# Performance work log

Hardware: AMD Instinct MI355X
Metric: run time of the kernel (lower is better)

## Reference

```python
import jax, jax.numpy as jnp
import numpy as np

B, D, L, N, M, K = 256, 512, 196, 1024, 512, 10000  # batch, context, num_ctx, hidden, embed, vocab


def setup_inputs() -> dict:
    key = jax.random.key(0)
    ks = jax.random.split(key, 20)
    r = lambda k, s: jax.random.normal(k, s, dtype=jnp.float32) * 0.02
    return {
        "a_i": jax.random.normal(ks[0], (B, D, L), dtype=jnp.float32),
        "inp": jax.random.normal(ks[1], (B, 1, K), dtype=jnp.float32),
        "hn_prev": jax.random.normal(ks[2], (B, 1, N), dtype=jnp.float32),
        "cn_prev": jax.random.normal(ks[3], (B, 1, N), dtype=jnp.float32),
        "f_att_w": r(ks[4], (N + D,)),  # Linear(n+D -> 1), stored as a vector
        "f_att_b": r(ks[5], (1,)),
        "gate_w": r(ks[6], (N,)),       # Linear(n -> 1)
        "gate_b": r(ks[7], (1,)),
        "E_w": r(ks[8], (M, K)),        # torch Linear weight [out, in]
        "E_b": r(ks[9], (M,)),
        "W_ih": r(ks[10], (4 * N, D + N + M)),  # LSTM input->hidden (i,f,g,o)
        "W_hh": r(ks[11], (4 * N, N)),
        "b_ih": r(ks[12], (4 * N,)),
        "b_hh": r(ks[13], (4 * N,)),
        "Lh_w": r(ks[14], (M, N)),
        "Lh_b": r(ks[15], (M,)),
        "Lz_w": r(ks[16], (M, D)),
        "Lz_b": r(ks[17], (M,)),
        "Lo_w": r(ks[18], (K, M)),
        "Lo_b": r(ks[19], (K,)),
    }


def reference(a_i, inp, hn_prev, cn_prev,
              f_att_w, f_att_b, gate_w, gate_b,
              E_w, E_b, W_ih, W_hh, b_ih, b_hh,
              Lh_w, Lh_b, Lz_w, Lz_b, Lo_w, Lo_b):
    h = hn_prev[:, 0]  # [B, N]
    c = cn_prev[:, 0]  # [B, N]
    # --- additive attention: the 196-iteration torch loop batched into one einsum ---
    # cat((a_i[:,:,i], h)) @ f_att_w splits into the a-part and h-part of the weight.
    w_a, w_h = f_att_w[:D], f_att_w[D:]
    e = jnp.einsum('bdl,d->bl', a_i, w_a) + (h @ w_h)[:, None] + f_att_b  # [B, L]
    alpha = jax.nn.softmax(e, axis=1)                                     # [B, L]
    beta = jax.nn.sigmoid(h @ gate_w + gate_b)                            # [B]
    z = beta[:, None] * jnp.einsum('bl,bdl->bd', alpha, a_i)              # [B, D]
    # --- word embedding ---
    w_emb = inp[:, 0] @ E_w.T + E_b                                       # [B, M]
    # --- single-step LSTM (PyTorch gate order i, f, g, o) ---
    x = jnp.concatenate([w_emb, h, z], axis=1)                            # [B, M+N+D]
    gates = x @ W_ih.T + b_ih + h @ W_hh.T + b_hh                         # [B, 4N]
    i_g, f_g, g_g, o_g = jnp.split(gates, 4, axis=1)
    cn = jax.nn.sigmoid(f_g) * c + jax.nn.sigmoid(i_g) * jnp.tanh(g_g)
    hn = jax.nn.sigmoid(o_g) * jnp.tanh(cn)
    # --- output projection ---
    deep_out = w_emb + (hn @ Lh_w.T + Lh_b) + (z @ Lz_w.T + Lz_b)         # [B, M]
    p_yt = deep_out @ Lo_w.T + Lo_b                                       # [B, K]
    return (p_yt[:, None, :], hn[:, None, :], cn[:, None, :], alpha[:, None, :])
```

## Files before the change

### kernel.cpp

```cpp
#include <hip/hip_runtime.h>
#include <hip/hip_bf16.h>
#include <math.h>

#define BB 256
#define DD 512
#define LL 196
#define NN 1024
#define MM 512
#define KK 10000

#define OUT_PY 0
#define OUT_HN ((size_t)2560000)
#define OUT_CN ((size_t)2822144)
#define OUT_AL ((size_t)3084288)

#define OFF_PE     ((size_t)0)
#define OFF_BETA   ((size_t)802816)
#define OFF_Z      ((size_t)803072)
#define OFF_EMB    ((size_t)934144)
#define OFF_DEEP   ((size_t)1065216)
#define OFF_EMBP   ((size_t)1196288)
#define OFF_GATESP ((size_t)2244864)
#define OFF_DP     ((size_t)10633472)

typedef __attribute__((ext_vector_type(8))) short short8v;
typedef __attribute__((ext_vector_type(4))) float f32x4;

__device__ __forceinline__ unsigned short f2bf(float f) {
    unsigned int u = __builtin_bit_cast(unsigned int, f);
    u += 0x7fffu + ((u >> 16) & 1u);
    return (unsigned short)(u >> 16);
}

__device__ __forceinline__ short8v stage8(const float* __restrict__ p, bool ok,
                                          int kbase, int Ktot) {
    short8v v;
    if (ok && (kbase + 7 < Ktot)) {
        const float4 x = *(const float4*)(p + kbase);
        const float4 y = *(const float4*)(p + kbase + 4);
        v[0] = (short)f2bf(x.x); v[1] = (short)f2bf(x.y);
        v[2] = (short)f2bf(x.z); v[3] = (short)f2bf(x.w);
        v[4] = (short)f2bf(y.x); v[5] = (short)f2bf(y.y);
        v[6] = (short)f2bf(y.z); v[7] = (short)f2bf(y.w);
    } else {
#pragma unroll
        for (int i = 0; i < 8; ++i) {
            const int k = kbase + i;
            v[i] = (short)f2bf((ok && k < Ktot) ? p[k] : 0.f);
        }
    }
    return v;
}

struct GSrc { const float* A; int lda; const float* B; int ldb; int ktn; int K; };

__device__ __forceinline__ void gemm_body(
    const int bx, const int by, const int bz, const int rowBlocks,
    const GSrc s1, const GSrc s2,
    float* __restrict__ C, const int ldc, const int Ncols,
    const int ktPerSplit, const float* __restrict__ bias,
    short (*As)[64][72], short (*Bs)[64][72])
{
    const int t = threadIdx.x;
    const int row0 = bx * 64;
    const int col0 = by * 64;
    const int ktTot = s1.ktn + s2.ktn;
    const int kt0 = bz * ktPerSplit;
    const int nk = min(ktTot, kt0 + ktPerSplit) - kt0;

    const int sr = t >> 2;
    const int sk = (t & 3) << 4;
    const int bc = col0 + sr;
    const bool bok = (bc < Ncols);
    const float* aP1 = s1.A + (size_t)(row0 + sr) * s1.lda;
    const float* bP1 = s1.B + (size_t)(bok ? bc : 0) * s1.ldb;
    const float* aP2 = s2.A ? (s2.A + (size_t)(row0 + sr) * s2.lda) : aP1;
    const float* bP2 = s2.A ? (s2.B + (size_t)(bok ? bc : 0) * s2.ldb) : bP1;

    const int l = t & 63, w = t >> 6;
    const int wrow = (w >> 1) * 32, wcol = (w & 1) * 32;
    const int lr = l & 15, g = l >> 4, g8 = g * 8;

    f32x4 acc[2][2] = {};

    short8v sa0, sa1, sb0, sb1;
    {
        const int ktg = kt0;
        const float* aR; const float* bR; int kk, Kt;
        if (ktg < s1.ktn) { aR = aP1; bR = bP1; kk = (ktg << 6) + sk; Kt = s1.K; }
        else              { aR = aP2; bR = bP2; kk = ((ktg - s1.ktn) << 6) + sk; Kt = s2.K; }
        sa0 = stage8(aR, true, kk, Kt);  sa1 = stage8(aR, true, kk + 8, Kt);
        sb0 = stage8(bR, bok,  kk, Kt);  sb1 = stage8(bR, bok,  kk + 8, Kt);
    }
    *(short8v*)&As[0][sr][sk] = sa0; *(short8v*)&As[0][sr][sk + 8] = sa1;
    *(short8v*)&Bs[0][sr][sk] = sb0; *(short8v*)&Bs[0][sr][sk + 8] = sb1;
    __syncthreads();

    int cur = 0;
    for (int kt = 0; kt < nk; ++kt) {
        const bool more = (kt + 1 < nk);
        if (more) {
            const int ktg = kt0 + kt + 1;
            const float* aR; const float* bR; int kk, Kt;
            if (ktg < s1.ktn) { aR = aP1; bR = bP1; kk = (ktg << 6) + sk; Kt = s1.K; }
            else              { aR = aP2; bR = bP2; kk = ((ktg - s1.ktn) << 6) + sk; Kt = s2.K; }
            sa0 = stage8(aR, true, kk, Kt);  sa1 = stage8(aR, true, kk + 8, Kt);
            sb0 = stage8(bR, bok,  kk, Kt);  sb1 = stage8(bR, bok,  kk + 8, Kt);
        }
#pragma unroll
        for (int ks = 0; ks < 2; ++ks) {
            const int ko = ks * 32 + g8;
            short8v a0 = *(const short8v*)&As[cur][wrow + lr][ko];
            short8v a1 = *(const short8v*)&As[cur][wrow + 16 + lr][ko];
            short8v b0 = *(const short8v*)&Bs[cur][wcol + lr][ko];
            short8v b1 = *(const short8v*)&Bs[cur][wcol + 16 + lr][ko];
            acc[0][0] = __builtin_amdgcn_mfma_f32_16x16x32_bf16(a0, b0, acc[0][0], 0, 0, 0);
            acc[0][1] = __builtin_amdgcn_mfma_f32_16x16x32_bf16(a0, b1, acc[0][1], 0, 0, 0);
            acc[1][0] = __builtin_amdgcn_mfma_f32_16x16x32_bf16(a1, b0, acc[1][0], 0, 0, 0);
            acc[1][1] = __builtin_amdgcn_mfma_f32_16x16x32_bf16(a1, b1, acc[1][1], 0, 0, 0);
        }
        if (more) {
            *(short8v*)&As[cur ^ 1][sr][sk] = sa0;
            *(short8v*)&As[cur ^ 1][sr][sk + 8] = sa1;
            *(short8v*)&Bs[cur ^ 1][sr][sk] = sb0;
            *(short8v*)&Bs[cur ^ 1][sr][sk + 8] = sb1;
        }
        __syncthreads();
        cur ^= 1;
    }

    float* Cp = C + (size_t)bz * ((size_t)rowBlocks * 64) * ldc;
#pragma unroll
    for (int m = 0; m < 2; ++m)
#pragma unroll
        for (int n = 0; n < 2; ++n)
#pragma unroll
            for (int j = 0; j < 4; ++j) {
                const int r = row0 + wrow + m * 16 + g * 4 + j;
                const int c = col0 + wcol + n * 16 + lr;
                if (c < Ncols) {
                    float v = acc[m][n][j];
                    if (bias) v += bias[c];
                    Cp[(size_t)r * ldc + c] = v;
                }
            }
}

__global__ __launch_bounds__(256) void k1_atte_emb_gatesh(
    const float* __restrict__ a_i, const float* __restrict__ f_att_w,
    float* __restrict__ pe,
    const float* __restrict__ inp, const float* __restrict__ E_w,
    float* __restrict__ embp,
    const float* __restrict__ h, const float* __restrict__ W_ih,
    const float* __restrict__ W_hh, float* __restrict__ gatesp)
{
    __shared__ __align__(16) unsigned char smem[36864];
    const int bid = blockIdx.x;
    const int t = threadIdx.x;

    if (bid < 4096) {
        float* pw = (float*)smem;
        const int b = bid >> 4, ch = bid & 15;
        const int w = t >> 6, lane = t & 63;
        const int d0 = ch * 32 + w * 8;
        const float* base = a_i + ((size_t)b * DD + d0) * LL;
        float e4[4] = {0.f, 0.f, 0.f, 0.f};
        if (lane < 49) {
            float4 rbuf[8];
#pragma unroll
            for (int i = 0; i < 8; ++i)
                rbuf[i] = *(const float4*)(base + (size_t)i * LL + lane * 4);
#pragma unroll
            for (int i = 0; i < 8; ++i) {
                const float wa = f_att_w[d0 + i];
                e4[0] += rbuf[i].x * wa; e4[1] += rbuf[i].y * wa;
                e4[2] += rbuf[i].z * wa; e4[3] += rbuf[i].w * wa;
            }
            *(float4*)&pw[w * 200 + lane * 4] = *(const float4*)e4;
        }
        __syncthreads();
        if (t < LL) {
            const float s = pw[t] + pw[200 + t] + pw[400 + t] + pw[600 + t];
            pe[((size_t)b * 16 + ch) * LL + t] = s;
        }
    } else if (bid < 4352) {
        short (*As)[64][72] = (short (*)[64][72])smem;
        short (*Bs)[64][72] = (short (*)[64][72])(smem + 18432);
        const int i = bid - 4096;
        GSrc s1 = {inp, KK, E_w, KK, 157, KK};
        GSrc s2 = {nullptr, 0, nullptr, 0, 0, 0};
        gemm_body(i & 3, (i >> 2) & 7, i >> 5, 4, s1, s2,
                  embp, MM, MM, 20, nullptr, As, Bs);
    } else {
        short (*As)[64][72] = (short (*)[64][72])smem;
        short (*Bs)[64][72] = (short (*)[64][72])(smem + 18432);
        const int i = bid - 4352;
        GSrc s1 = {h, NN, W_ih + 512, 2048, 16, NN};
        GSrc s2 = {h, NN, W_hh, NN, 16, NN};
        gemm_body(i & 3, (i >> 2) & 63, i >> 8, 4, s1, s2,
                  gatesp, 4096, 4096, 8, nullptr, As, Bs);
    }
}

__global__ __launch_bounds__(256) void k2_softmax_embred(
    const float* __restrict__ pe, const float* __restrict__ h,
    const float* __restrict__ f_att_w, const float* __restrict__ f_att_b,
    const float* __restrict__ gate_w, const float* __restrict__ gate_b,
    float* __restrict__ alpha_out, float* __restrict__ beta,
    const float* __restrict__ embp, const float* __restrict__ E_b,
    float* __restrict__ emb)
{
    const int bid = blockIdx.x;
    const int t = threadIdx.x;
    if (bid < 256) {
        const int b = bid;
        __shared__ float red[256];
        __shared__ float red2[256];
        const float4 h4 = *(const float4*)(h + (size_t)b * NN + t * 4);
        const float4 w4 = *(const float4*)(f_att_w + DD + t * 4);
        const float4 g4 = *(const float4*)(gate_w + t * 4);
        float hd = h4.x * w4.x + h4.y * w4.y + h4.z * w4.z + h4.w * w4.w;
        float gd = h4.x * g4.x + h4.y * g4.y + h4.z * g4.z + h4.w * g4.w;
        red[t] = hd; red2[t] = gd;
        __syncthreads();
        for (int s = 128; s > 0; s >>= 1) {
            if (t < s) { red[t] += red[t + s]; red2[t] += red2[t + s]; }
            __syncthreads();
        }
        const float hdot = red[0];
        const float gdot = red2[0];
        __syncthreads();
        float e = -3.4e38f;
        if (t < LL) {
            const float* p = pe + (size_t)b * 16 * LL + t;
            e = hdot + f_att_b[0];
#pragma unroll
            for (int ch = 0; ch < 16; ++ch) e += p[ch * LL];
        }
        red[t] = e;
        __syncthreads();
        for (int s = 128; s > 0; s >>= 1) {
            if (t < s) red[t] = fmaxf(red[t], red[t + s]);
            __syncthreads();
        }
        const float mx = red[0];
        __syncthreads();
        const float ex = (t < LL) ? expf(e - mx) : 0.f;
        red[t] = ex;
        __syncthreads();
        for (int s = 128; s > 0; s >>= 1) {
            if (t < s) red[t] += red[t + s];
            __syncthreads();
        }
        const float inv = 1.f / red[0];
        if (t < LL) alpha_out[(size_t)b * LL + t] = ex * inv;
        if (t == 0) beta[b] = 1.f / (1.f + expf(-(gdot + gate_b[0])));
    } else {
        const int idx = (bid - 256) * 256 + t;
        const int j = idx & 511;
        float v = E_b[j];
#pragma unroll
        for (int s = 0; s < 8; ++s) v += embp[(size_t)s * (BB * 512) + idx];
        emb[idx] = v;
    }
}

__global__ __launch_bounds__(256) void k3_attz_gatese(
    const float* __restrict__ a_i, const float* __restrict__ alpha,
    const float* __restrict__ beta, float* __restrict__ z,
    const float* __restrict__ emb, const float* __restrict__ W_ih,
    float* __restrict__ gatesp_e)
{
    __shared__ __align__(16) unsigned char smem[36864];
    const int bid = blockIdx.x;
    const int t = threadIdx.x;

    if (bid < 4096) {
        float* al = (float*)smem;
        const int b = bid >> 4, ch = bid & 15;
        const int w = t >> 6, lane = t & 63;
        if (t < LL) al[t] = alpha[(size_t)b * LL + t];
        __syncthreads();
        const int d0 = ch * 32 + w * 8;
        const float* base = a_i + ((size_t)b * DD + d0) * LL;
        const float bet = beta[b];
        float4 av = make_float4(0.f, 0.f, 0.f, 0.f);
        float4 rbuf[8];
        if (lane < 49) {
            av = *(const float4*)&al[lane * 4];
#pragma unroll
            for (int i = 0; i < 8; ++i)
                rbuf[i] = *(const float4*)(base + (size_t)i * LL + lane * 4);
        }
#pragma unroll
        for (int i = 0; i < 8; ++i) {
            float s = (lane < 49) ? (rbuf[i].x * av.x + rbuf[i].y * av.y +
                                     rbuf[i].z * av.z + rbuf[i].w * av.w) : 0.f;
#pragma unroll
            for (int off = 32; off > 0; off >>= 1) s += __shfl_down(s, off, 64);
            if (lane == 0) z[(size_t)b * DD + d0 + i] = bet * s;
        }
    } else {
        short (*As)[64][72] = (short (*)[64][72])smem;
        short (*Bs)[64][72] = (short (*)[64][72])(smem + 18432);
        const int i = bid - 4096;
        GSrc s1 = {emb, MM, W_ih, 2048, 8, MM};
        GSrc s2 = {nullptr, 0, nullptr, 0, 0, 0};
        gemm_body(i & 3, (i >> 2) & 63, i >> 8, 4, s1, s2,
                  gatesp_e, 4096, 4096, 4, nullptr, As, Bs);
    }
}

__global__ __launch_bounds__(256) void k4_gatesz_lz(
    const float* __restrict__ z, const float* __restrict__ W_ih,
    float* __restrict__ gatesp_z,
    const float* __restrict__ Lz_w, float* __restrict__ dp)
{
    __shared__ __align__(16) unsigned char smem[36864];
    short (*As)[64][72] = (short (*)[64][72])smem;
    short (*Bs)[64][72] = (short (*)[64][72])(smem + 18432);
    const int bid = blockIdx.x;
    if (bid < 512) {
        GSrc s1 = {z, DD, W_ih + 1536, 2048, 8, DD};
        GSrc s2 = {nullptr, 0, nullptr, 0, 0, 0};
        gemm_body(bid & 3, (bid >> 2) & 63, bid >> 8, 4, s1, s2,
                  gatesp_z, 4096, 4096, 4, nullptr, As, Bs);
    } else {
        const int i = bid - 512;
        GSrc s1 = {z, DD, Lz_w, DD, 8, DD};
        GSrc s2 = {nullptr, 0, nullptr, 0, 0, 0};
        gemm_body(i & 3, (i >> 2) & 7, i >> 5, 4, s1, s2,
                  dp, MM, MM, 1, nullptr, As, Bs);
    }
}

__global__ __launch_bounds__(256) void k5_lstm(
    const float* __restrict__ gatesp,
    const float* __restrict__ b_ih, const float* __restrict__ b_hh,
    const float* __restrict__ c_prev, float* __restrict__ hn, float* __restrict__ cn)
{
    const int idx = blockIdx.x * 256 + threadIdx.x;
    const int b = idx >> 10, n = idx & 1023;
    float g[4];
#pragma unroll
    for (int gi = 0; gi < 4; ++gi) {
        const int col = gi * 1024 + n;
        const size_t o = (size_t)b * 4096 + col;
        float v = b_ih[col] + b_hh[col];
#pragma unroll
        for (int s = 0; s < 8; ++s) v += gatesp[(size_t)s * (BB * 4096) + o];
        g[gi] = v;
    }
    const float si = 1.f / (1.f + expf(-g[0]));
    const float sf = 1.f / (1.f + expf(-g[1]));
    const float so = 1.f / (1.f + expf(-g[3]));
    const float tg = tanhf(g[2]);
    const float c = c_prev[idx];
    const float cnv = sf * c + si * tg;
    const float hnv = so * tanhf(cnv);
    cn[idx] = cnv;
    hn[idx] = hnv;
}

__global__ __launch_bounds__(256) void k6_lh(
    const float* __restrict__ hn, const float* __restrict__ Lh_w,
    float* __restrict__ dp_hi)
{
    __shared__ __align__(16) unsigned char smem[36864];
    short (*As)[64][72] = (short (*)[64][72])smem;
    short (*Bs)[64][72] = (short (*)[64][72])(smem + 18432);
    const int bid = blockIdx.x;
    GSrc s1 = {hn, NN, Lh_w, NN, 16, NN};
    GSrc s2 = {nullptr, 0, nullptr, 0, 0, 0};
    gemm_body(bid & 3, (bid >> 2) & 7, bid >> 5, 4, s1, s2,
              dp_hi, MM, MM, 1, nullptr, As, Bs);
}

__global__ __launch_bounds__(256) void k7_deep(
    const float* __restrict__ emb, const float* __restrict__ dp,
    const float* __restrict__ Lh_b, const float* __restrict__ Lz_b,
    float* __restrict__ deep)
{
    const int idx = blockIdx.x * 256 + threadIdx.x;
    const int j = idx & 511;
    float v = emb[idx] + Lh_b[j] + Lz_b[j];
#pragma unroll
    for (int s = 0; s < 24; ++s) v += dp[(size_t)s * (BB * 512) + idx];
    deep[idx] = v;
}

__global__ __launch_bounds__(256) void k8_pyt(
    const float* __restrict__ deep, const float* __restrict__ Lo_w,
    const float* __restrict__ Lo_b, float* __restrict__ out)
{
    __shared__ __align__(16) unsigned char smem[36864];
    short (*As)[64][72] = (short (*)[64][72])smem;
    short (*Bs)[64][72] = (short (*)[64][72])(smem + 18432);
    const int bid = blockIdx.x;
    GSrc s1 = {deep, MM, Lo_w, MM, 8, MM};
    GSrc s2 = {nullptr, 0, nullptr, 0, 0, 0};
    gemm_body(bid & 3, bid >> 2, 0, 4, s1, s2,
              out, KK, KK, 8, Lo_b, As, Bs);
}

extern "C" void kernel_launch(void* const* d_in, const int* in_sizes, int n_in,
                              void* d_out, int out_size, void* d_ws, size_t ws_size,
                              hipStream_t stream)
{
    const float* a_i     = (const float*)d_in[0];
    const float* inp     = (const float*)d_in[1];
    const float* hn_prev = (const float*)d_in[2];
    const float* cn_prev = (const float*)d_in[3];
    const float* f_att_w = (const float*)d_in[4];
    const float* f_att_b = (const float*)d_in[5];
    const float* gate_w  = (const float*)d_in[6];
    const float* gate_b  = (const float*)d_in[7];
    const float* E_w     = (const float*)d_in[8];
    const float* E_b     = (const float*)d_in[9];
    const float* W_ih    = (const float*)d_in[10];
    const float* W_hh    = (const float*)d_in[11];
    const float* b_ih    = (const float*)d_in[12];
    const float* b_hh    = (const float*)d_in[13];
    const float* Lh_w    = (const float*)d_in[14];
    const float* Lh_b    = (const float*)d_in[15];
    const float* Lz_w    = (const float*)d_in[16];
    const float* Lz_b    = (const float*)d_in[17];
    const float* Lo_w    = (const float*)d_in[18];
    const float* Lo_b    = (const float*)d_in[19];

    float* out = (float*)d_out;
    float* ws  = (float*)d_ws;

    float* PE     = ws + OFF_PE;
    float* BETA   = ws + OFF_BETA;
    float* Z      = ws + OFF_Z;
    float* EMB    = ws + OFF_EMB;
    float* DEEP   = ws + OFF_DEEP;
    float* EMBP   = ws + OFF_EMBP;
    float* GATESP = ws + OFF_GATESP;
    float* DP     = ws + OFF_DP;

    k1_atte_emb_gatesh<<<5376, 256, 0, stream>>>(
        a_i, f_att_w, PE, inp, E_w, EMBP, hn_prev, W_ih, W_hh, GATESP);

    k2_softmax_embred<<<768, 256, 0, stream>>>(PE, hn_prev, f_att_w, f_att_b,
                                               gate_w, gate_b, out + OUT_AL, BETA,
                                               EMBP, E_b, EMB);

    k3_attz_gatese<<<4608, 256, 0, stream>>>(a_i, out + OUT_AL, BETA, Z,
                                             EMB, W_ih,
                                             GATESP + (size_t)4 * BB * 4096);

    k4_gatesz_lz<<<768, 256, 0, stream>>>(Z, W_ih,
                                          GATESP + (size_t)6 * BB * 4096,
                                          Lz_w, DP);

    k5_lstm<<<1024, 256, 0, stream>>>(GATESP, b_ih, b_hh, cn_prev,
                                      out + OUT_HN, out + OUT_CN);

    k6_lh<<<512, 256, 0, stream>>>(out + OUT_HN, Lh_w,
                                   DP + (size_t)8 * BB * 512);

    k7_deep<<<512, 256, 0, stream>>>(EMB, DP, Lh_b, Lz_b, DEEP);

    k8_pyt<<<628, 256, 0, stream>>>(DEEP, Lo_w, Lo_b, out + OUT_PY);
}
```

Baseline: 156.3 us.

## Stage a_i chunks in LDS, deepen GEMM prefetch, rebalance embedding split-K

The attention-score and context kernels now copy a 64×196 slab of a_i into LDS with coalesced float4 loads and reduce from shared memory. This replaces the per-wave strided float4 loads that left lanes idle, and halves the number of partial-score chunks. The shared GEMM body gets a two-deep register prefetch using ping-pong register sets. The embedding GEMM moves from 8 to 32 split-K slices, so there are more blocks but more partial sums for k2 to reduce. The LDS footprint grows to about 51 KB per block, which may lower occupancy for every block of these kernels, including the GEMM ones.

```diff
diff --git a/kernel.cpp b/kernel.cpp
--- a/kernel.cpp
+++ b/kernel.cpp
@@ -15,13 +15,13 @@
 #define OUT_AL ((size_t)3084288)
 
 #define OFF_PE     ((size_t)0)
-#define OFF_BETA   ((size_t)802816)
-#define OFF_Z      ((size_t)803072)
-#define OFF_EMB    ((size_t)934144)
-#define OFF_DEEP   ((size_t)1065216)
-#define OFF_EMBP   ((size_t)1196288)
-#define OFF_GATESP ((size_t)2244864)
-#define OFF_DP     ((size_t)10633472)
+#define OFF_BETA   ((size_t)401408)
+#define OFF_Z      ((size_t)401664)
+#define OFF_EMB    ((size_t)532736)
+#define OFF_DEEP   ((size_t)663808)
+#define OFF_EMBP   ((size_t)794880)
+#define OFF_GATESP ((size_t)4989184)
+#define OFF_DP     ((size_t)13377792)
 
 typedef __attribute__((ext_vector_type(8))) short short8v;
 typedef __attribute__((ext_vector_type(4))) float f32x4;
@@ -81,52 +81,54 @@
     const int wrow = (w >> 1) * 32, wcol = (w & 1) * 32;
     const int lr = l & 15, g = l >> 4, g8 = g * 8;
 
+#define GLOAD(ktg, sa0_, sa1_, sb0_, sb1_)                                     \
+    {                                                                          \
+        const float* aR; const float* bR; int kk, Kt;                          \
+        if ((ktg) < s1.ktn) { aR = aP1; bR = bP1; kk = ((ktg) << 6) + sk; Kt = s1.K; } \
+        else { aR = aP2; bR = bP2; kk = (((ktg) - s1.ktn) << 6) + sk; Kt = s2.K; } \
+        sa0_ = stage8(aR, true, kk, Kt);  sa1_ = stage8(aR, true, kk + 8, Kt); \
+        sb0_ = stage8(bR, bok,  kk, Kt);  sb1_ = stage8(bR, bok,  kk + 8, Kt); \
+    }
+#define GSTORE(buf, sa0_, sa1_, sb0_, sb1_)                                    \
+    {                                                                          \
+        *(short8v*)&As[buf][sr][sk] = sa0_; *(short8v*)&As[buf][sr][sk + 8] = sa1_; \
+        *(short8v*)&Bs[buf][sr][sk] = sb0_; *(short8v*)&Bs[buf][sr][sk + 8] = sb1_; \
+    }
+#define GMFMA(buf)                                                             \
+    _Pragma("unroll")                                                          \
+    for (int ks = 0; ks < 2; ++ks) {                                           \
+        const int ko = ks * 32 + g8;                                           \
+        short8v a0 = *(const short8v*)&As[buf][wrow + lr][ko];                 \
+        short8v a1 = *(const short8v*)&As[buf][wrow + 16 + lr][ko];            \
+        short8v b0 = *(const short8v*)&Bs[buf][wcol + lr][ko];                 \
+        short8v b1 = *(const short8v*)&Bs[buf][wcol + 16 + lr][ko];            \
+        acc[0][0] = __builtin_amdgcn_mfma_f32_16x16x32_bf16(a0, b0, acc[0][0], 0, 0, 0); \
+        acc[0][1] = __builtin_amdgcn_mfma_f32_16x16x32_bf16(a0, b1, acc[0][1], 0, 0, 0); \
+        acc[1][0] = __builtin_amdgcn_mfma_f32_16x16x32_bf16(a1, b0, acc[1][0], 0, 0, 0); \
+        acc[1][1] = __builtin_amdgcn_mfma_f32_16x16x32_bf16(a1, b1, acc[1][1], 0, 0, 0); \
+    }
+
     f32x4 acc[2][2] = {};
-
-    short8v sa0, sa1, sb0, sb1;
-    {
-        const int ktg = kt0;
-        const float* aR; const float* bR; int kk, Kt;
-        if (ktg < s1.ktn) { aR = aP1; bR = bP1; kk = (ktg << 6) + sk; Kt = s1.K; }
-        else              { aR = aP2; bR = bP2; kk = ((ktg - s1.ktn) << 6) + sk; Kt = s2.K; }
-        sa0 = stage8(aR, true, kk, Kt);  sa1 = stage8(aR, true, kk + 8, Kt);
-        sb0 = stage8(bR, bok,  kk, Kt);  sb1 = stage8(bR, bok,  kk + 8, Kt);
-    }
-    *(short8v*)&As[0][sr][sk] = sa0; *(short8v*)&As[0][sr][sk + 8] = sa1;
-    *(short8v*)&Bs[0][sr][sk] = sb0; *(short8v*)&Bs[0][sr][sk + 8] = sb1;
+    short8v Aa0, Aa1, Ab0, Ab1;
+    short8v Ba0, Ba1, Bb0, Bb1;
+
+    GLOAD(kt0, Aa0, Aa1, Ab0, Ab1);
+    GSTORE(0, Aa0, Aa1, Ab0, Ab1);
+    if (nk > 1) GLOAD(kt0 + 1, Aa0, Aa1, Ab0, Ab1);
     __syncthreads();
 
-    int cur = 0;
-    for (int kt = 0; kt < nk; ++kt) {
-        const bool more = (kt + 1 < nk);
-        if (more) {
-            const int ktg = kt0 + kt + 1;
-            const float* aR; const float* bR; int kk, Kt;
-            if (ktg < s1.ktn) { aR = aP1; bR = bP1; kk = (ktg << 6) + sk; Kt = s1.K; }
-            else              { aR = aP2; bR = bP2; kk = ((ktg - s1.ktn) << 6) + sk; Kt = s2.K; }
-            sa0 = stage8(aR, true, kk, Kt);  sa1 = stage8(aR, true, kk + 8, Kt);
-            sb0 = stage8(bR, bok,  kk, Kt);  sb1 = stage8(bR, bok,  kk + 8, Kt);
-        }
-#pragma unroll
-        for (int ks = 0; ks < 2; ++ks) {
-            const int ko = ks * 32 + g8;
-            short8v a0 = *(const short8v*)&As[cur][wrow + lr][ko];
-            short8v a1 = *(const short8v*)&As[cur][wrow + 16 + lr][ko];
-            short8v b0 = *(const short8v*)&Bs[cur][wcol + lr][ko];
-            short8v b1 = *(const short8v*)&Bs[cur][wcol + 16 + lr][ko];
-            acc[0][0] = __builtin_amdgcn_mfma_f32_16x16x32_bf16(a0, b0, acc[0][0], 0, 0, 0);
-            acc[0][1] = __builtin_amdgcn_mfma_f32_16x16x32_bf16(a0, b1, acc[0][1], 0, 0, 0);
-            acc[1][0] = __builtin_amdgcn_mfma_f32_16x16x32_bf16(a1, b0, acc[1][0], 0, 0, 0);
-            acc[1][1] = __builtin_amdgcn_mfma_f32_16x16x32_bf16(a1, b1, acc[1][1], 0, 0, 0);
-        }
-        if (more) {
-            *(short8v*)&As[cur ^ 1][sr][sk] = sa0;
-            *(short8v*)&As[cur ^ 1][sr][sk + 8] = sa1;
-            *(short8v*)&Bs[cur ^ 1][sr][sk] = sb0;
-            *(short8v*)&Bs[cur ^ 1][sr][sk + 8] = sb1;
-        }
-        __syncthreads();
-        cur ^= 1;
+    int cur = 0, kt = 0;
+    while (true) {
+        if (kt + 2 < nk) GLOAD(kt0 + kt + 2, Ba0, Ba1, Bb0, Bb1);
+        GMFMA(cur);
+        if (kt + 1 < nk) GSTORE(cur ^ 1, Aa0, Aa1, Ab0, Ab1);
+        __syncthreads();
+        cur ^= 1; if (++kt >= nk) break;
+        if (kt + 2 < nk) GLOAD(kt0 + kt + 2, Aa0, Aa1, Ab0, Ab1);
+        GMFMA(cur);
+        if (kt + 1 < nk) GSTORE(cur ^ 1, Ba0, Ba1, Bb0, Bb1);
+        __syncthreads();
+        cur ^= 1; if (++kt >= nk) break;
     }
 
     float* Cp = C + (size_t)bz * ((size_t)rowBlocks * 64) * ldc;
@@ -144,6 +146,9 @@
                     Cp[(size_t)r * ldc + c] = v;
                 }
             }
+#undef GLOAD
+#undef GSTORE
+#undef GMFMA
 }
 
 __global__ __launch_bounds__(256) void k1_atte_emb_gatesh(
@@ -154,47 +159,38 @@
     const float* __restrict__ h, const float* __restrict__ W_ih,
     const float* __restrict__ W_hh, float* __restrict__ gatesp)
 {
-    __shared__ __align__(16) unsigned char smem[36864];
+    __shared__ __align__(16) unsigned char smem[52224];
     const int bid = blockIdx.x;
     const int t = threadIdx.x;
 
-    if (bid < 4096) {
-        float* pw = (float*)smem;
-        const int b = bid >> 4, ch = bid & 15;
-        const int w = t >> 6, lane = t & 63;
-        const int d0 = ch * 32 + w * 8;
-        const float* base = a_i + ((size_t)b * DD + d0) * LL;
-        float e4[4] = {0.f, 0.f, 0.f, 0.f};
-        if (lane < 49) {
-            float4 rbuf[8];
-#pragma unroll
-            for (int i = 0; i < 8; ++i)
-                rbuf[i] = *(const float4*)(base + (size_t)i * LL + lane * 4);
-#pragma unroll
-            for (int i = 0; i < 8; ++i) {
-                const float wa = f_att_w[d0 + i];
-                e4[0] += rbuf[i].x * wa; e4[1] += rbuf[i].y * wa;
-                e4[2] += rbuf[i].z * wa; e4[3] += rbuf[i].w * wa;
-            }
-            *(float4*)&pw[w * 200 + lane * 4] = *(const float4*)e4;
-        }
+    if (bid < 2048) {
+        float* lds = (float*)smem;
+        const int b = bid >> 3, ch = bid & 7;
+        const float4* g4 = (const float4*)(a_i + ((size_t)b * DD + ch * 64) * LL);
+        float4* l4 = (float4*)lds;
+#pragma unroll
+        for (int i = 0; i < 12; ++i) l4[t + i * 256] = g4[t + i * 256];
+        if (t < 64) l4[t + 3072] = g4[t + 3072];
         __syncthreads();
         if (t < LL) {
-            const float s = pw[t] + pw[200 + t] + pw[400 + t] + pw[600 + t];
-            pe[((size_t)b * 16 + ch) * LL + t] = s;
-        }
-    } else if (bid < 4352) {
+            const float* wp = f_att_w + ch * 64;
+            float e = 0.f;
+#pragma unroll 16
+            for (int d = 0; d < 64; ++d) e += lds[d * LL + t] * wp[d];
+            pe[((size_t)b * 8 + ch) * LL + t] = e;
+        }
+    } else if (bid < 3072) {
         short (*As)[64][72] = (short (*)[64][72])smem;
         short (*Bs)[64][72] = (short (*)[64][72])(smem + 18432);
-        const int i = bid - 4096;
+        const int i = bid - 2048;
         GSrc s1 = {inp, KK, E_w, KK, 157, KK};
         GSrc s2 = {nullptr, 0, nullptr, 0, 0, 0};
         gemm_body(i & 3, (i >> 2) & 7, i >> 5, 4, s1, s2,
-                  embp, MM, MM, 20, nullptr, As, Bs);
+                  embp, MM, MM, 5, nullptr, As, Bs);
     } else {
         short (*As)[64][72] = (short (*)[64][72])smem;
         short (*Bs)[64][72] = (short (*)[64][72])(smem + 18432);
-        const int i = bid - 4352;
+        const int i = bid - 3072;
         GSrc s1 = {h, NN, W_ih + 512, 2048, 16, NN};
         GSrc s2 = {h, NN, W_hh, NN, 16, NN};
         gemm_body(i & 3, (i >> 2) & 63, i >> 8, 4, s1, s2,
@@ -232,10 +228,10 @@
         __syncthreads();
         float e = -3.4e38f;
         if (t < LL) {
-            const float* p = pe + (size_t)b * 16 * LL + t;
+            const float* p = pe + (size_t)b * 8 * LL + t;
             e = hdot + f_att_b[0];
 #pragma unroll
-            for (int ch = 0; ch < 16; ++ch) e += p[ch * LL];
+            for (int ch = 0; ch < 8; ++ch) e += p[ch * LL];
         }
         red[t] = e;
         __syncthreads();
@@ -260,7 +256,7 @@
         const int j = idx & 511;
         float v = E_b[j];
 #pragma unroll
-        for (int s = 0; s < 8; ++s) v += embp[(size_t)s * (BB * 512) + idx];
+        for (int s = 0; s < 32; ++s) v += embp[(size_t)s * (BB * 512) + idx];
         emb[idx] = v;
     }
 }
@@ -271,39 +267,34 @@
     const float* __restrict__ emb, const float* __restrict__ W_ih,
     float* __restrict__ gatesp_e)
 {
-    __shared__ __align__(16) unsigned char smem[36864];
+    __shared__ __align__(16) unsigned char smem[52224];
     const int bid = blockIdx.x;
     const int t = threadIdx.x;
 
-    if (bid < 4096) {
-        float* al = (float*)smem;
-        const int b = bid >> 4, ch = bid & 15;
-        const int w = t >> 6, lane = t & 63;
+    if (bid < 2048) {
+        float* lds = (float*)smem;
+        float* al  = lds + 64 * LL;
+        const int b = bid >> 3, ch = bid & 7;
+        const float4* g4 = (const float4*)(a_i + ((size_t)b * DD + ch * 64) * LL);
+        float4* l4 = (float4*)lds;
+#pragma unroll
+        for (int i = 0; i < 12; ++i) l4[t + i * 256] = g4[t + i * 256];
+        if (t < 64) l4[t + 3072] = g4[t + 3072];
         if (t < LL) al[t] = alpha[(size_t)b * LL + t];
         __syncthreads();
-        const int d0 = ch * 32 + w * 8;
-        const float* base = a_i + ((size_t)b * DD + d0) * LL;
-        const float bet = beta[b];
-        float4 av = make_float4(0.f, 0.f, 0.f, 0.f);
-        float4 rbuf[8];
-        if (lane < 49) {
-            av = *(const float4*)&al[lane * 4];
-#pragma unroll
-            for (int i = 0; i < 8; ++i)
-                rbuf[i] = *(const float4*)(base + (size_t)i * LL + lane * 4);
-        }
-#pragma unroll
-        for (int i = 0; i < 8; ++i) {
-            float s = (lane < 49) ? (rbuf[i].x * av.x + rbuf[i].y * av.y +
-                                     rbuf[i].z * av.z + rbuf[i].w * av.w) : 0.f;
-#pragma unroll
-            for (int off = 32; off > 0; off >>= 1) s += __shfl_down(s, off, 64);
-            if (lane == 0) z[(size_t)b * DD + d0 + i] = bet * s;
-        }
+        const int r = t >> 2, q = t & 3;
+        const float* rowp = lds + r * LL + q * 49;
+        const float* alq  = al + q * 49;
+        float s = 0.f;
+#pragma unroll 7
+        for (int j = 0; j < 49; ++j) s += rowp[j] * alq[j];
+        s += __shfl_xor(s, 1, 64);
+        s += __shfl_xor(s, 2, 64);
+        if (q == 0) z[(size_t)b * DD + ch * 64 + r] = beta[b] * s;
     } else {
         short (*As)[64][72] = (short (*)[64][72])smem;
         short (*Bs)[64][72] = (short (*)[64][72])(smem + 18432);
-        const int i = bid - 4096;
+        const int i = bid - 2048;
         GSrc s1 = {emb, MM, W_ih, 2048, 8, MM};
         GSrc s2 = {nullptr, 0, nullptr, 0, 0, 0};
         gemm_body(i & 3, (i >> 2) & 63, i >> 8, 4, s1, s2,
@@ -440,14 +431,14 @@
     float* GATESP = ws + OFF_GATESP;
     float* DP     = ws + OFF_DP;
 
-    k1_atte_emb_gatesh<<<5376, 256, 0, stream>>>(
+    k1_atte_emb_gatesh<<<4096, 256, 0, stream>>>(
         a_i, f_att_w, PE, inp, E_w, EMBP, hn_prev, W_ih, W_hh, GATESP);
 
     k2_softmax_embred<<<768, 256, 0, stream>>>(PE, hn_prev, f_att_w, f_att_b,
                                                gate_w, gate_b, out + OUT_AL, BETA,
                                                EMBP, E_b, EMB);
 
-    k3_attz_gatese<<<4608, 256, 0, stream>>>(a_i, out + OUT_AL, BETA, Z,
+    k3_attz_gatese<<<2560, 256, 0, stream>>>(a_i, out + OUT_AL, BETA, Z,
                                              EMB, W_ih,
                                              GATESP + (size_t)4 * BB * 4096);
 
```

Result: slower. 165.1 us (+5.6%).
